# Kernel tuning notes

Hardware: AMD Instinct MI355X
Metric: run time of the kernel (lower is better)

Reference implementation:

```python
import jax, jax.numpy as jnp
import numpy as np

B, C, N, HID = 1, 64, 1024, 128


def setup_inputs() -> dict:
    key = jax.random.key(0)
    k1, k2, k3, k4, k5 = jax.random.split(key, 5)
    x = jax.random.normal(k1, (B, C, N), dtype=jnp.float32)
    # Conv2d(2C -> HID, 1): weight [HID, 2C] (1x1 kernel flattened), bias [HID]
    W1 = jax.random.normal(k2, (HID, 2 * C), dtype=jnp.float32) * (1.0 / np.sqrt(2 * C))
    b1 = jax.random.normal(k3, (HID,), dtype=jnp.float32) * 0.01
    # Conv2d(HID -> 1, 1): weight [HID], bias [1]
    W2 = jax.random.normal(k4, (HID,), dtype=jnp.float32) * (1.0 / np.sqrt(HID))
    b2 = jax.random.normal(k5, (1,), dtype=jnp.float32) * 0.01
    return {"x": x, "W1": W1, "b1": b1, "W2": W2, "b2": b2}


def reference(x, W1, b1, W2, b2):
    # Original: m1[b,c,i,j] = x[b,c,j]; m2[b,c,i,j] = x[b,c,i]; block = cat([m1, m2], dim=1)
    # tanh is elementwise, and the 1x1 conv is linear, so we split W1 into the
    # halves acting on m1 (j-indexed) and m2 (i-indexed) and avoid the explicit
    # O(N^2 * 2C) repeat+concat. The nonlinear hidden tensor [B,HID,N,N] is the
    # same math as Conv2d(tanh(block)).
    c = x.shape[1]
    t = jnp.tanh(x)                                   # [B, C, N]
    pj = jnp.einsum('hc,bcn->bhn', W1[:, :c], t)      # contribution of m1 (varies over j)
    pi = jnp.einsum('hc,bcn->bhn', W1[:, c:], t)      # contribution of m2 (varies over i)
    h = jnp.tanh(pi[:, :, :, None] + pj[:, :, None, :] + b1[None, :, None, None])  # [B,HID,N,N]
    e = jnp.einsum('h,bhij->bij', W2, h) + b2[0]      # [B, N, N]
    return e + jnp.swapaxes(e, 1, 2)
```

## Files before the change

kernel.cpp:

```cpp
#include <hip/hip_runtime.h>
#include <math.h>

#define CN    64
#define NN    1024
#define NPAIR 528
#define NCHUNK 8

__device__ __forceinline__ float tanh_fast(float x) {
    float e = __expf(2.0f * x);
    return 1.0f - 2.0f * __builtin_amdgcn_rcpf(e + 1.0f);
}

__global__ __launch_bounds__(256) void prep_kernel(
    const float* __restrict__ x, const float* __restrict__ W1,
    const float* __restrict__ b1, float2* __restrict__ S)
{
    __shared__ float t_s[2][64];
    const int tid = threadIdx.x;
    const int n0  = blockIdx.x * 2;

    if (tid < 64) {
        float2 xv = *(const float2*)&x[tid * NN + n0];
        t_s[0][tid] = tanh_fast(xv.x);
        t_s[1][tid] = tanh_fast(xv.y);
    }
    __syncthreads();

    const int h  = tid & 127;
    const int nl = tid >> 7;
    const float4* wrow = (const float4*)(W1 + h * (2 * CN));

    float pj[4] = {0.f, 0.f, 0.f, 0.f};
    float pi[4] = {0.f, 0.f, 0.f, 0.f};
#pragma unroll
    for (int c4 = 0; c4 < 16; ++c4) {
        float4 tv = *(const float4*)&t_s[nl][c4 * 4];
        float4 wl = wrow[c4];
        float4 wh = wrow[16 + c4];
        const int s = c4 & 3;
        pj[s] = fmaf(wl.x, tv.x, fmaf(wl.y, tv.y, fmaf(wl.z, tv.z, fmaf(wl.w, tv.w, pj[s]))));
        pi[s] = fmaf(wh.x, tv.x, fmaf(wh.y, tv.y, fmaf(wh.z, tv.z, fmaf(wh.w, tv.w, pi[s]))));
    }
    float pjs = (pj[0] + pj[1]) + (pj[2] + pj[3]);
    float pis = (pi[0] + pi[1]) + (pi[2] + pi[3]);
    float U = tanh_fast(pis + b1[h]);
    float V = tanh_fast(pjs);
    S[h * NN + n0 + nl] = make_float2(U, V);
}

__global__ __launch_bounds__(64) void pair_kernel(
    const float2* __restrict__ S, const float* __restrict__ W2,
    float* __restrict__ ws)
{
    const int id = blockIdx.x;
    const int pair = id >> 3, chunk = id & 7;
    int r = (int)((sqrtf(8.f * pair + 1.f) - 1.f) * 0.5f);
    while ((r + 1) * (r + 2) / 2 <= pair) ++r;
    while (r * (r + 1) / 2 > pair) --r;
    const int bi = pair - r * (r + 1) / 2, bj = r;
    const int i0 = bi * 32, j0 = bj * 32, h0 = chunk * 16;

    __shared__ float2 Si[16 * 32];
    __shared__ float2 Sj[16 * 32];
    const int lane = threadIdx.x;

    {
        float4* SiF = (float4*)Si;
        float4* SjF = (float4*)Sj;
        const float4* SF = (const float4*)S;
#pragma unroll
        for (int k = 0; k < 4; ++k) {
            int t = k * 64 + lane;
            int row = t >> 4, seg = t & 15;
            SiF[t] = SF[(((h0 + row) * NN + i0) >> 1) + seg];
            SjF[t] = SF[(((h0 + row) * NN + j0) >> 1) + seg];
        }
    }
    __syncthreads();

    const int la = lane & 7, lb = lane >> 3;
    float acc[4][4];
#pragma unroll
    for (int m = 0; m < 4; ++m)
#pragma unroll
        for (int n = 0; n < 4; ++n) acc[m][n] = 0.f;

#pragma unroll 4
    for (int h = 0; h < 16; ++h) {
        const float w2h = W2[h0 + h];
        float2 A[4], B[4];
#pragma unroll
        for (int m = 0; m < 4; ++m) A[m] = Si[h * 32 + la + 8 * m];
#pragma unroll
        for (int n = 0; n < 4; ++n) B[n] = Sj[h * 32 + lb + 8 * n];
        float PA[4], QA[4], PB[4], QB[4];
#pragma unroll
        for (int m = 0; m < 4; ++m) {
            PA[m] = w2h * (A[m].x + A[m].y);
            QA[m] = fmaf(A[m].x, A[m].y, 1.0f);
        }
#pragma unroll
        for (int n = 0; n < 4; ++n) {
            PB[n] = w2h * (B[n].x + B[n].y);
            QB[n] = fmaf(B[n].x, B[n].y, 1.0f);
        }
#pragma unroll
        for (int m = 0; m < 4; ++m)
#pragma unroll
            for (int n = 0; n < 4; ++n) {
                float d1 = fmaf(A[m].x, B[n].y, 1.0f);
                float d2 = fmaf(B[n].x, A[m].y, 1.0f);
                float rr = __builtin_amdgcn_rcpf(d1 * d2);
                float Np = fmaf(PA[m], QB[n], PB[n] * QA[m]);
                acc[m][n] = fmaf(Np, rr, acc[m][n]);
            }
    }

    float* wsp = ws + (pair * NCHUNK + chunk) * 1024;
#pragma unroll
    for (int m = 0; m < 4; ++m)
#pragma unroll
        for (int n = 0; n < 4; ++n)
            wsp[(m * 4 + n) * 64 + lane] = acc[m][n];
}

__global__ __launch_bounds__(256) void combine_kernel(
    const float* __restrict__ ws, const float* __restrict__ b2,
    float* __restrict__ out)
{
    const int pair = blockIdx.x;
    int r = (int)((sqrtf(8.f * pair + 1.f) - 1.f) * 0.5f);
    while ((r + 1) * (r + 2) / 2 <= pair) ++r;
    while (r * (r + 1) / 2 > pair) --r;
    const int bi = pair - r * (r + 1) / 2, bj = r;
    const int i0 = bi * 32, j0 = bj * 32;

    __shared__ float T[32 * 35];
    const int t = threadIdx.x;
    const int lane_p = t & 63, q0 = t >> 6;
    const int la = lane_p & 7, lb = (lane_p >> 3) & 7;
    const float bias2 = 2.0f * b2[0];
    const float* wsp = ws + pair * NCHUNK * 1024;

#pragma unroll
    for (int k = 0; k < 4; ++k) {
        float a = 0.f;
#pragma unroll
        for (int cc = 0; cc < NCHUNK; ++cc)
            a += wsp[cc * 1024 + (q0 + 4 * k) * 64 + lane_p];
        T[(la + 8 * k) * 35 + lb + 8 * q0] = a + bias2;
    }
    __syncthreads();

    const int tx = t & 15, ty = t >> 4;
#pragma unroll
    for (int k = 0; k < 4; ++k) {
        int rr2 = ty + (k >> 1) * 16;
        int cc2 = tx + (k & 1) * 16;
        out[(i0 + rr2) * NN + j0 + cc2] = T[rr2 * 35 + cc2];
    }
    if (bi != bj) {
#pragma unroll
        for (int k = 0; k < 4; ++k) {
            int rr2 = ty + (k >> 1) * 16;
            int cc2 = tx + (k & 1) * 16;
            out[(j0 + rr2) * NN + i0 + cc2] = T[cc2 * 35 + rr2];
        }
    }
}

extern "C" void kernel_launch(void* const* d_in, const int* in_sizes, int n_in,
                              void* d_out, int out_size, void* d_ws, size_t ws_size,
                              hipStream_t stream)
{
    const float* x  = (const float*)d_in[0];
    const float* W1 = (const float*)d_in[1];
    const float* b1 = (const float*)d_in[2];
    const float* W2 = (const float*)d_in[3];
    const float* b2 = (const float*)d_in[4];
    float* out = (float*)d_out;

    float2* S   = (float2*)d_ws;
    float*  par = (float*)((char*)d_ws + (size_t)2 * 1024 * 1024);

    prep_kernel<<<512, 256, 0, stream>>>(x, W1, b1, S);
    pair_kernel<<<NPAIR * NCHUNK, 64, 0, stream>>>(S, W2, par);
    combine_kernel<<<NPAIR, 256, 0, stream>>>(par, b2, out);
}
```

Before: 100.9 us.

## Fuse pair and combine kernels with in-block hidden-dim reduction

Merges the pair and combine kernels into one. Each 256-thread block now handles a full 32x32 tile pair, with its four waves splitting the 128 hidden channels and reducing their partials through shared memory. This removes the global partial-sum workspace round trip and one kernel launch. In exchange it uses 64KB of LDS per block, which lowers occupancy, and cuts the grid from 4224 to 528 blocks, which may underfill the GPU.

```diff
diff --git a/kernel.cpp b/kernel.cpp
--- a/kernel.cpp
+++ b/kernel.cpp
@@ -4,7 +4,6 @@
 #define CN    64
 #define NN    1024
 #define NPAIR 528
-#define NCHUNK 8
 
 __device__ __forceinline__ float tanh_fast(float x) {
     float e = __expf(2.0f * x);
@@ -48,59 +47,58 @@
     S[h * NN + n0 + nl] = make_float2(U, V);
 }
 
-__global__ __launch_bounds__(64) void pair_kernel(
+__global__ __launch_bounds__(256) void pair_kernel(
     const float2* __restrict__ S, const float* __restrict__ W2,
-    float* __restrict__ ws)
+    const float* __restrict__ b2, float* __restrict__ out)
 {
-    const int id = blockIdx.x;
-    const int pair = id >> 3, chunk = id & 7;
+    const int pair = blockIdx.x;
     int r = (int)((sqrtf(8.f * pair + 1.f) - 1.f) * 0.5f);
     while ((r + 1) * (r + 2) / 2 <= pair) ++r;
     while (r * (r + 1) / 2 > pair) --r;
     const int bi = pair - r * (r + 1) / 2, bj = r;
-    const int i0 = bi * 32, j0 = bj * 32, h0 = chunk * 16;
+    const int i0 = bi * 32, j0 = bj * 32;
 
-    __shared__ float2 Si[16 * 32];
-    __shared__ float2 Sj[16 * 32];
-    const int lane = threadIdx.x;
+    __shared__ float4 sm4[4096];
+    const int tid = threadIdx.x;
 
     {
-        float4* SiF = (float4*)Si;
-        float4* SjF = (float4*)Sj;
         const float4* SF = (const float4*)S;
+        const int ci = i0 >> 1, cj = j0 >> 1;
 #pragma unroll
-        for (int k = 0; k < 4; ++k) {
-            int t = k * 64 + lane;
-            int row = t >> 4, seg = t & 15;
-            SiF[t] = SF[(((h0 + row) * NN + i0) >> 1) + seg];
-            SjF[t] = SF[(((h0 + row) * NN + j0) >> 1) + seg];
+        for (int k = 0; k < 8; ++k) {
+            int idx = k * 256 + tid;
+            int h = idx >> 4, seg = idx & 15;
+            sm4[idx]        = SF[h * 512 + ci + seg];
+            sm4[2048 + idx] = SF[h * 512 + cj + seg];
         }
     }
     __syncthreads();
 
+    const int w = tid >> 6, lane = tid & 63;
     const int la = lane & 7, lb = lane >> 3;
-    float acc[4][4];
+    const float2* Si = (const float2*)sm4;
+    const float2* Sj = (const float2*)(sm4 + 2048);
+
+    float acc[16];
 #pragma unroll
-    for (int m = 0; m < 4; ++m)
-#pragma unroll
-        for (int n = 0; n < 4; ++n) acc[m][n] = 0.f;
+    for (int q = 0; q < 16; ++q) acc[q] = 0.f;
 
+    const int hbase = w * 32;
 #pragma unroll 4
-    for (int h = 0; h < 16; ++h) {
-        const float w2h = W2[h0 + h];
+    for (int hh = 0; hh < 32; ++hh) {
+        const int h = hbase + hh;
+        const float w2h = W2[h];
         float2 A[4], B[4];
-#pragma unroll
-        for (int m = 0; m < 4; ++m) A[m] = Si[h * 32 + la + 8 * m];
-#pragma unroll
-        for (int n = 0; n < 4; ++n) B[n] = Sj[h * 32 + lb + 8 * n];
         float PA[4], QA[4], PB[4], QB[4];
 #pragma unroll
         for (int m = 0; m < 4; ++m) {
+            A[m]  = Si[h * 32 + la + 8 * m];
             PA[m] = w2h * (A[m].x + A[m].y);
             QA[m] = fmaf(A[m].x, A[m].y, 1.0f);
         }
 #pragma unroll
         for (int n = 0; n < 4; ++n) {
+            B[n]  = Sj[h * 32 + lb + 8 * n];
             PB[n] = w2h * (B[n].x + B[n].y);
             QB[n] = fmaf(B[n].x, B[n].y, 1.0f);
         }
@@ -111,60 +109,44 @@
                 float d1 = fmaf(A[m].x, B[n].y, 1.0f);
                 float d2 = fmaf(B[n].x, A[m].y, 1.0f);
                 float rr = __builtin_amdgcn_rcpf(d1 * d2);
-                float Np = fmaf(PA[m], QB[n], PB[n] * QA[m]);
-                acc[m][n] = fmaf(Np, rr, acc[m][n]);
+                float Np = fmaf(PB[n], QA[m], PA[m] * QB[n]);
+                acc[m * 4 + n] = fmaf(Np, rr, acc[m * 4 + n]);
             }
     }
 
-    float* wsp = ws + (pair * NCHUNK + chunk) * 1024;
+    __syncthreads();
+    float* buf = (float*)sm4;
 #pragma unroll
-    for (int m = 0; m < 4; ++m)
-#pragma unroll
-        for (int n = 0; n < 4; ++n)
-            wsp[(m * 4 + n) * 64 + lane] = acc[m][n];
-}
+    for (int q = 0; q < 16; ++q)
+        buf[w * 1024 + q * 64 + lane] = acc[q];
+    __syncthreads();
 
-__global__ __launch_bounds__(256) void combine_kernel(
-    const float* __restrict__ ws, const float* __restrict__ b2,
-    float* __restrict__ out)
-{
-    const int pair = blockIdx.x;
-    int r = (int)((sqrtf(8.f * pair + 1.f) - 1.f) * 0.5f);
-    while ((r + 1) * (r + 2) / 2 <= pair) ++r;
-    while (r * (r + 1) / 2 > pair) --r;
-    const int bi = pair - r * (r + 1) / 2, bj = r;
-    const int i0 = bi * 32, j0 = bj * 32;
-
-    __shared__ float T[32 * 35];
-    const int t = threadIdx.x;
-    const int lane_p = t & 63, q0 = t >> 6;
-    const int la = lane_p & 7, lb = (lane_p >> 3) & 7;
+    float* T = (float*)(sm4 + 1024);
     const float bias2 = 2.0f * b2[0];
-    const float* wsp = ws + pair * NCHUNK * 1024;
-
 #pragma unroll
     for (int k = 0; k < 4; ++k) {
-        float a = 0.f;
-#pragma unroll
-        for (int cc = 0; cc < NCHUNK; ++cc)
-            a += wsp[cc * 1024 + (q0 + 4 * k) * 64 + lane_p];
-        T[(la + 8 * k) * 35 + lb + 8 * q0] = a + bias2;
+        int c  = tid + k * 256;
+        int q  = c >> 6, l2 = c & 63;
+        int m = q >> 2, n = q & 3;
+        int il = (l2 & 7) + 8 * m, jl = (l2 >> 3) + 8 * n;
+        float v = buf[c] + buf[1024 + c] + buf[2048 + c] + buf[3072 + c] + bias2;
+        T[il * 34 + jl] = v;
     }
     __syncthreads();
 
-    const int tx = t & 15, ty = t >> 4;
+    const int tx = tid & 15, ty = tid >> 4;
 #pragma unroll
     for (int k = 0; k < 4; ++k) {
         int rr2 = ty + (k >> 1) * 16;
         int cc2 = tx + (k & 1) * 16;
-        out[(i0 + rr2) * NN + j0 + cc2] = T[rr2 * 35 + cc2];
+        out[(i0 + rr2) * NN + j0 + cc2] = T[rr2 * 34 + cc2];
     }
     if (bi != bj) {
 #pragma unroll
         for (int k = 0; k < 4; ++k) {
             int rr2 = ty + (k >> 1) * 16;
             int cc2 = tx + (k & 1) * 16;
-            out[(j0 + rr2) * NN + i0 + cc2] = T[cc2 * 35 + rr2];
+            out[(j0 + rr2) * NN + i0 + cc2] = T[cc2 * 34 + rr2];
         }
     }
 }
@@ -179,11 +161,8 @@
     const float* W2 = (const float*)d_in[3];
     const float* b2 = (const float*)d_in[4];
     float* out = (float*)d_out;
-
-    float2* S   = (float2*)d_ws;
-    float*  par = (float*)((char*)d_ws + (size_t)2 * 1024 * 1024);
+    float2* S  = (float2*)d_ws;
 
     prep_kernel<<<512, 256, 0, stream>>>(x, W1, b1, S);
-    pair_kernel<<<NPAIR * NCHUNK, 64, 0, stream>>>(S, W2, par);
-    combine_kernel<<<NPAIR, 256, 0, stream>>>(par, b2, out);
+    pair_kernel<<<NPAIR, 256, 0, stream>>>(S, W2, b2, out);
 }
```

After: 95.66 us. 5.2% less time.
